# Optimization experiments

Measured on AMD Instinct MI355X. Metric: run time of the kernel, lower is better.

## Reference

```python
import jax, jax.numpy as jnp
import numpy as np

K_GIBBS = 1
LR = 0.01


def _sample_binary(key, probs):
    # relu(sign(p - u)) == 1 iff p > u, else 0
    u = jax.random.uniform(key, probs.shape, dtype=probs.dtype)
    return (probs > u).astype(probs.dtype)


def setup_inputs() -> dict:
    key = jax.random.key(0)
    k1, k2 = jax.random.split(key)
    B, H, Wd, C, hid = 64, 64, 64, 3, 4096
    flat = H * Wd * C  # 12288
    inputs = jax.random.uniform(k1, (B, H, Wd, C), dtype=jnp.float32)
    W = 0.1 * jax.random.normal(k2, (flat, hid), dtype=jnp.float32)  # stddev=0.1 as in build()
    a = jnp.zeros((flat,), jnp.float32)
    b = jnp.zeros((hid,), jnp.float32)
    return {"inputs": inputs, "W": W, "a": a, "b": b}


def reference(inputs, W, a, b):
    B, H, Wd, C = inputs.shape
    flat = H * Wd * C
    vs = inputs.reshape(B, flat)
    keys = jax.random.split(jax.random.key(42), B)
    h0 = jnp.zeros((W.shape[1],), dtype=W.dtype)

    def step(carry, xb):
        W, a, b, h = carry
        v0, key = xb
        kbin, kinit = jax.random.split(key)
        # k Gibbs sampling steps: h = sig(b + W^T v); v = sig(a + W h)
        v = v0
        for _ in range(K_GIBBS):
            h = jax.nn.sigmoid(b + W.T @ v)
            v = jax.nn.sigmoid(a + W @ h)
        # contrastive divergence (rank-1 updates)
        h_bin = _sample_binary(kbin, h)
        h_init = _sample_binary(kinit, jax.nn.sigmoid(b + W.T @ v0))
        W = W + LR * (jnp.outer(v0, h_init) - jnp.outer(v, h_bin))
        a = a + LR * (v0 - v)
        b = b + LR * (h_init - h_bin)
        return (W, a, b, h), None

    (Wf, af, bf, hf), _ = jax.lax.scan(step, (W, a, b, h0), (vs, keys))
    # final self.v.assign(self.v_given_h()) with updated params and last h
    v_final = jax.nn.sigmoid(af + Wf @ hf)
    return v_final.reshape(H, Wd, C)
```

## Files before the change

kernel.cpp:

```cpp
#include <hip/hip_runtime.h>
#include <stdint.h>
#include <math.h>


#define NB   64
#define FLAT 12288
#define HID  4096
#define LRf  0.01f
#define LRd  0.01
#define RNG_MODE 0

#define OFF_KEYS   0u
#define OFF_B      1024u
#define OFF_A      17408u
#define OFF_H      66560u
#define OFF_ALP    82944u
#define OFF_BEP    91136u
#define OFF_G0     99328u
#define OFF_GV     132096u
#define OFF_HIB    164864u
#define OFF_HBB    197632u
#define OFF_C      230400u
#define OFF_V      1278976u
#define OFF_VT     4424704u
#define OFF_V0T    7570432u
#define OFF_HIBC   10716160u
#define OFF_HBBC   10748928u
#define OFF_CPART  1278976u
#define NCH 6

__device__ __forceinline__ void tf(uint32_t k0, uint32_t k1,
                                   uint32_t x0, uint32_t x1,
                                   uint32_t& o0, uint32_t& o1) {
  uint32_t ks[3] = {k0, k1, k0 ^ k1 ^ 0x1BD11BDAu};
  x0 += ks[0]; x1 += ks[1];
  const int R0[4] = {13, 15, 26, 6};
  const int R1[4] = {17, 29, 16, 24};
#pragma unroll
  for (int i = 0; i < 5; ++i) {
    const int* r = (i & 1) ? R1 : R0;
#pragma unroll
    for (int q = 0; q < 4; ++q) {
      x0 += x1;
      x1 = (x1 << r[q]) | (x1 >> (32 - r[q]));
      x1 ^= x0;
    }
    x0 += ks[(i + 1) % 3];
    x1 += ks[(i + 2) % 3] + (uint32_t)(i + 1);
  }
  o0 = x0; o1 = x1;
}

__device__ __forceinline__ float u01(uint32_t bits) {
  uint32_t fb = (bits >> 9) | 0x3f800000u;
  return __uint_as_float(fb) - 1.0f;
}

__global__ void k_setup(const float* a_in, const float* b_in,
                        float* a_cur, float* b_cur, uint32_t* keys4) {
  int gid = blockIdx.x * blockDim.x + threadIdx.x;
  int stride = gridDim.x * blockDim.x;
  for (int i = gid; i < FLAT; i += stride) a_cur[i] = a_in[i];
  for (int i = gid; i < HID; i += stride) b_cur[i] = b_in[i];
  if (gid < NB) {
    uint32_t t = (uint32_t)gid;
    uint32_t kt0, kt1, o0, o1, p0, p1;
#if RNG_MODE == 0
    tf(0u, 42u, 0u, t, kt0, kt1);
    tf(kt0, kt1, 0u, 0u, o0, o1);
    tf(kt0, kt1, 0u, 1u, p0, p1);
    keys4[4 * gid + 0] = o0; keys4[4 * gid + 1] = o1;
    keys4[4 * gid + 2] = p0; keys4[4 * gid + 3] = p1;
#else
    if (t < 32) {
      tf(0u, 42u, 2 * t,     64 + 2 * t, o0, o1); kt0 = o0;
      tf(0u, 42u, 2 * t + 1, 65 + 2 * t, o0, o1); kt1 = o0;
    } else {
      tf(0u, 42u, 2 * t - 64, 2 * t,     o0, o1); kt0 = o1;
      tf(0u, 42u, 2 * t - 63, 2 * t + 1, o0, o1); kt1 = o1;
    }
    uint32_t a0, a1, b0, b1;
    tf(kt0, kt1, 0u, 2u, a0, a1);
    tf(kt0, kt1, 1u, 3u, b0, b1);
    keys4[4 * gid + 0] = a0; keys4[4 * gid + 1] = b0;
    keys4[4 * gid + 2] = a1; keys4[4 * gid + 3] = b1;
#endif
  }
}

__global__ void k_vt(const float* v0all, float* v0T) {
  int i = blockIdx.x * 256 + threadIdx.x;
#pragma unroll 8
  for (int s = 0; s < NB; ++s)
    v0T[(size_t)i * NB + s] = v0all[(size_t)s * FLAT + i];
}

__global__ __launch_bounds__(256) void k_g0(const float* v0all, double* G0) {
  const int t = blockIdx.x, s = blockIdx.y;
  const float4* vs = (const float4*)(v0all + (size_t)s * FLAT);
  const float4* vt = (const float4*)(v0all + (size_t)t * FLAT);
  double acc = 0.0;
  for (int e = threadIdx.x; e < FLAT / 4; e += 256) {
    float4 a = vs[e], b = vt[e];
    acc += (double)a.x * b.x + (double)a.y * b.y +
           (double)a.z * b.z + (double)a.w * b.w;
  }
  for (int m = 32; m; m >>= 1) acc += __shfl_xor(acc, m, 64);
  __shared__ double red[4];
  int wv = threadIdx.x >> 6, lane = threadIdx.x & 63;
  if (lane == 0) red[wv] = acc;
  __syncthreads();
  if (threadIdx.x == 0) G0[s * NB + t] = red[0] + red[1] + red[2] + red[3];
}

__global__ __launch_bounds__(256) void k_cgemm(const float* v0T, const float* W0,
                                               float* Cpart) {
  const int jl = threadIdx.x & 63;
  const int tth = threadIdx.x >> 6;
  const int j0 = blockIdx.x * 64;
  const int ilen = FLAT / NCH;
  const int ibeg = blockIdx.y * ilen, iend = ibeg + ilen;
  __shared__ float lv[64 * 68];
  __shared__ float lw[64 * 68];
  float acc[16];
#pragma unroll
  for (int k = 0; k < 16; ++k) acc[k] = 0.f;
  for (int i0 = ibeg; i0 < iend; i0 += 64) {
    __syncthreads();
    const float4* vsrc = (const float4*)(v0T + (size_t)i0 * NB);
#pragma unroll
    for (int k = 0; k < 4; ++k) {
      int f = threadIdx.x + k * 256;
      int row = f >> 4, c4 = f & 15;
      *(float4*)(&lv[row * 68 + c4 * 4]) = vsrc[f];
    }
#pragma unroll
    for (int k = 0; k < 4; ++k) {
      int f = threadIdx.x + k * 256;
      int row = f >> 4, c4 = f & 15;
      *(float4*)(&lw[row * 68 + c4 * 4]) =
          *(const float4*)(W0 + (size_t)(i0 + row) * HID + j0 + c4 * 4);
    }
    __syncthreads();
#pragma unroll 2
    for (int ii = 0; ii < 64; ++ii) {
      float w = lw[ii * 68 + jl];
      const float* lp = &lv[ii * 68 + tth * 16];
#pragma unroll
      for (int k4 = 0; k4 < 4; ++k4) {
        float4 hv = *(const float4*)(lp + 4 * k4);
        acc[4 * k4 + 0] += w * hv.x;
        acc[4 * k4 + 1] += w * hv.y;
        acc[4 * k4 + 2] += w * hv.z;
        acc[4 * k4 + 3] += w * hv.w;
      }
    }
  }
#pragma unroll
  for (int k = 0; k < 16; ++k)
    Cpart[((size_t)blockIdx.y * NB + tth * 16 + k) * HID + j0 + jl] = acc[k];
}

__global__ void k_creduce(const float* Cpart, float* C) {
  int gid = blockIdx.x * blockDim.x + threadIdx.x;
  if (gid >= NB * HID) return;
  double s = 0.0;
  for (int c = 0; c < NCH; ++c) s += (double)Cpart[(size_t)c * NB * HID + gid];
  C[gid] = (float)s;
}

__global__ __launch_bounds__(256) void k_hbc(int t, const float* Call,
                                             const double* G0, const double* GV,
                                             float* b_cur, float* h_cur,
                                             uint32_t* Hib, uint32_t* Hbb,
                                             uint64_t* HibC, uint64_t* HbbC,
                                             double* alp, double* bep,
                                             const uint32_t* keys4) {
  const int tid = threadIdx.x;
  const int lane = tid & 63, wv = tid >> 6;
  const int j = blockIdx.x * 256 + tid;
  __shared__ double g0c[NB], gvc[NB];
  __shared__ float h_blk[256];
  __shared__ unsigned char ib_blk[256], bb_blk[256];
  __shared__ uint32_t ldsI[NB][8], ldsB[NB][8];
  for (int s = tid; s < NB; s += 256) { g0c[s] = G0[s * NB + t]; gvc[s] = GV[s * NB + t]; }
  for (int idx = tid; idx < t * 8; idx += 256) {
    int s = idx >> 3, w = idx & 7;
    ldsI[s][w] = Hib[s * 128 + blockIdx.x * 8 + w];
    ldsB[s][w] = Hbb[s * 128 + blockIdx.x * 8 + w];
  }
  __syncthreads();
  uint64_t rawI = (t == 0) ? 0ull : HibC[j];
  uint64_t rawB = (t == 0) ? 0ull : HbbC[j];
  const uint64_t mlow = (t == 0) ? 0ull : ((1ull << t) - 1ull);
  uint64_t mi64 = rawI & mlow, mb64 = rawB & mlow;
  double accp = 0.0, accm = 0.0;
  while (mi64) { int s = __builtin_ctzll(mi64); accp += g0c[s]; mi64 &= mi64 - 1; }
  while (mb64) { int s = __builtin_ctzll(mb64); accm += gvc[s]; mb64 &= mb64 - 1; }
  double lg = (double)b_cur[j] + (double)Call[(size_t)t * HID + j] + LRd * (accp - accm);
  float h = (float)(1.0 / (1.0 + exp(-lg)));
  h_cur[j] = h;
  uint32_t o0, o1;
  uint32_t kb0 = keys4[4 * t], kb1 = keys4[4 * t + 1];
  uint32_t ki0 = keys4[4 * t + 2], ki1 = keys4[4 * t + 3];
#if RNG_MODE == 0
  tf(kb0, kb1, 0u, (uint32_t)j, o0, o1); float ub = u01(o0 ^ o1);
  tf(ki0, ki1, 0u, (uint32_t)j, o0, o1); float ui = u01(o0 ^ o1);
#else
  uint32_t m = (uint32_t)(j & (HID / 2 - 1));
  tf(kb0, kb1, m, m + HID / 2, o0, o1); float ub = u01(j < HID / 2 ? o0 : o1);
  tf(ki0, ki1, m, m + HID / 2, o0, o1); float ui = u01(j < HID / 2 ? o0 : o1);
#endif
  bool hb = h > ub, hi = h > ui;
  unsigned long long mb = __ballot(hb), mi = __ballot(hi);
  const int word = j >> 5;
  if (lane == 0) {
    Hbb[t * 128 + word]     = (uint32_t)mb;
    Hbb[t * 128 + word + 1] = (uint32_t)(mb >> 32);
    Hib[t * 128 + word]     = (uint32_t)mi;
    Hib[t * 128 + word + 1] = (uint32_t)(mi >> 32);
  }
  HibC[j] = rawI | ((uint64_t)(hi ? 1 : 0) << t);
  HbbC[j] = rawB | ((uint64_t)(hb ? 1 : 0) << t);
  b_cur[j] += LRf * ((hi ? 1.f : 0.f) - (hb ? 1.f : 0.f));
  h_blk[tid] = h; ib_blk[tid] = hi ? 1 : 0; bb_blk[tid] = hb ? 1 : 0;
  __syncthreads();
  for (int task = wv; task < 2 * (t + 1); task += 4) {
    int s = task >> 1;
    const bool useB = task & 1;
    double p = 0.0;
#pragma unroll
    for (int q = 0; q < 4; ++q) {
      int jj = q * 64 + lane;
      bool on;
      if (s == t) on = (useB ? bb_blk[jj] : ib_blk[jj]) != 0;
      else {
        uint32_t w32 = useB ? ldsB[s][jj >> 5] : ldsI[s][jj >> 5];
        on = (w32 >> (jj & 31)) & 1u;
      }
      if (on) p += (double)h_blk[jj];
    }
    for (int m2 = 32; m2; m2 >>= 1) p += __shfl_xor(p, m2, 64);
    if (lane == 0) {
      if (useB) bep[(size_t)blockIdx.x * NB + s] = p;
      else      alp[(size_t)blockIdx.x * NB + s] = p;
    }
  }
}

__global__ __launch_bounds__(512) void k_gemv(int t, const float* W0,
                                              const float* v0T, const float* h_cur,
                                              const double* alp, const double* bep,
                                              float* a_cur, float* V, float* Vt,
                                              float* out) {
  __shared__ float hs[HID];
  __shared__ double als[NB], bes[NB];
  const int tid = threadIdx.x;
  for (int e = tid; e < HID / 4; e += 512)
    ((float4*)hs)[e] = ((const float4*)h_cur)[e];
  if (tid < NB) {
    double asum = 0.0, bsum = 0.0;
#pragma unroll
    for (int b = 0; b < 16; ++b) {
      asum += alp[(size_t)b * NB + tid];
      bsum += bep[(size_t)b * NB + tid];
    }
    als[tid] = asum; bes[tid] = bsum;
  }
  __syncthreads();
  const int wv = tid >> 6, lane = tid & 63;
  const int row = blockIdx.x * 8 + wv;
  const float4* wr = (const float4*)(W0 + (size_t)row * HID);
  double acc = 0.0;
#pragma unroll
  for (int c = 0; c < 16; ++c) {
    float4 w = wr[c * 64 + lane];
    float4 hh = ((const float4*)hs)[c * 64 + lane];
    acc += (double)w.x * hh.x + (double)w.y * hh.y +
           (double)w.z * hh.z + (double)w.w * hh.w;
  }
  const int smax = (t > NB - 1) ? NB : t;
  if (lane < smax) {
    double c = (double)v0T[(size_t)row * NB + lane] * als[lane]
             - (double)Vt[(size_t)row * NB + lane] * bes[lane];
    acc += LRd * c;
  }
  for (int m = 32; m; m >>= 1) acc += __shfl_xor(acc, m, 64);
  if (lane == 0) {
    double lg = (double)a_cur[row] + acc;
    float v = (float)(1.0 / (1.0 + exp(-lg)));
    if (t == NB) {
      out[row] = v;
    } else {
      V[(size_t)t * FLAT + row] = v;
      Vt[(size_t)row * NB + t] = v;
      a_cur[row] += LRf * (v0T[(size_t)row * NB + t] - v);
    }
  }
}

__global__ void k_gv(int t, const float* v0all, const float* V, double* GV) {
  int tp = t + 1 + blockIdx.x;
  const float4* vt = (const float4*)(V + (size_t)t * FLAT);
  const float4* v0 = (const float4*)(v0all + (size_t)tp * FLAT);
  double acc = 0.0;
  for (int e = threadIdx.x; e < FLAT / 4; e += 256) {
    float4 a = vt[e], b = v0[e];
    acc += (double)a.x * b.x + (double)a.y * b.y +
           (double)a.z * b.z + (double)a.w * b.w;
  }
  for (int m = 32; m; m >>= 1) acc += __shfl_xor(acc, m, 64);
  __shared__ double red[4];
  int wv = threadIdx.x >> 6, lane = threadIdx.x & 63;
  if (lane == 0) red[wv] = acc;
  __syncthreads();
  if (threadIdx.x == 0) GV[t * NB + tp] = red[0] + red[1] + red[2] + red[3];
}

extern "C" void kernel_launch(void* const* d_in, const int* in_sizes, int n_in,
                              void* d_out, int out_size, void* d_ws, size_t ws_size,
                              hipStream_t stream) {
  const float* inputs = (const float*)d_in[0];
  const float* W0     = (const float*)d_in[1];
  const float* a_in   = (const float*)d_in[2];
  const float* b_in   = (const float*)d_in[3];
  float* out = (float*)d_out;

  char* ws = (char*)d_ws;
  uint32_t* keys4 = (uint32_t*)(ws + OFF_KEYS);
  float* b_cur = (float*)(ws + OFF_B);
  float* a_cur = (float*)(ws + OFF_A);
  float* h_cur = (float*)(ws + OFF_H);
  double* alp  = (double*)(ws + OFF_ALP);
  double* bep  = (double*)(ws + OFF_BEP);
  double* G0   = (double*)(ws + OFF_G0);
  double* GV   = (double*)(ws + OFF_GV);
  uint32_t* Hib = (uint32_t*)(ws + OFF_HIB);
  uint32_t* Hbb = (uint32_t*)(ws + OFF_HBB);
  uint64_t* HibC = (uint64_t*)(ws + OFF_HIBC);
  uint64_t* HbbC = (uint64_t*)(ws + OFF_HBBC);
  float* C     = (float*)(ws + OFF_C);
  float* V     = (float*)(ws + OFF_V);
  float* Vt    = (float*)(ws + OFF_VT);
  float* v0T   = (float*)(ws + OFF_V0T);
  float* Cpart = (float*)(ws + OFF_CPART);

  hipLaunchKernelGGL(k_setup, dim3(48), dim3(256), 0, stream,
                     a_in, b_in, a_cur, b_cur, keys4);
  hipLaunchKernelGGL(k_g0, dim3(NB, NB), dim3(256), 0, stream, inputs, G0);
  hipLaunchKernelGGL(k_vt, dim3(FLAT / 256), dim3(256), 0, stream, inputs, v0T);
  hipLaunchKernelGGL(k_cgemm, dim3(HID / 64, NCH), dim3(256), 0, stream,
                     v0T, W0, Cpart);
  hipLaunchKernelGGL(k_creduce, dim3((NB * HID + 255) / 256), dim3(256), 0,
                     stream, Cpart, C);

  for (int t = 0; t < NB; ++t) {
    hipLaunchKernelGGL(k_hbc, dim3(HID / 256), dim3(256), 0, stream,
                       t, C, G0, GV, b_cur, h_cur, Hib, Hbb, HibC, HbbC,
                       alp, bep, keys4);
    hipLaunchKernelGGL(k_gemv, dim3(FLAT / 8), dim3(512), 0, stream,
                       t, W0, v0T, h_cur, alp, bep, a_cur, V, Vt, out);
    if (t < NB - 1)
      hipLaunchKernelGGL(k_gv, dim3(NB - 1 - t), dim3(256), 0, stream,
                         t, inputs, V, GV);
  }
  hipLaunchKernelGGL(k_gemv, dim3(FLAT / 8), dim3(512), 0, stream,
                     NB, W0, v0T, h_cur, alp, bep, a_cur, V, Vt, out);
}
```

Baseline: 4.042 ms.

## Fuse GV dot products into gemv epilogue and reduce partials in k_hbc

Removes the per-step k_gv kernel. k_gemv now computes per-block partial products of the new v with every v0 column and writes them to Gpart. The next k_hbc reduces those partials into GV and gvc, which saves one launch per step and a separate full reread of V and the inputs. It also retiles k_cgemm to 32-column tiles with 8 accumulators and raises NCH to 8, giving more blocks. The cost is extra shared memory and a syncthreads in gemv, plus a 1536-entry column reduction done redundantly inside each k_hbc block.

```diff
diff --git a/kernel.cpp b/kernel.cpp
--- a/kernel.cpp
+++ b/kernel.cpp
@@ -9,6 +9,7 @@
 #define LRf  0.01f
 #define LRd  0.01
 #define RNG_MODE 0
+#define GEMV_BLOCKS (FLAT / 8)
 
 #define OFF_KEYS   0u
 #define OFF_B      1024u
@@ -21,13 +22,13 @@
 #define OFF_HIB    164864u
 #define OFF_HBB    197632u
 #define OFF_C      230400u
-#define OFF_V      1278976u
 #define OFF_VT     4424704u
 #define OFF_V0T    7570432u
 #define OFF_HIBC   10716160u
 #define OFF_HBBC   10748928u
-#define OFF_CPART  1278976u
-#define NCH 6
+#define OFF_CPART  10781696u
+#define NCH 8
+#define OFF_GPART  19170304u
 
 __device__ __forceinline__ void tf(uint32_t k0, uint32_t k1,
                                    uint32_t x0, uint32_t x1,
@@ -115,16 +116,16 @@
 
 __global__ __launch_bounds__(256) void k_cgemm(const float* v0T, const float* W0,
                                                float* Cpart) {
-  const int jl = threadIdx.x & 63;
-  const int tth = threadIdx.x >> 6;
-  const int j0 = blockIdx.x * 64;
+  const int jl = threadIdx.x & 31;
+  const int tth = threadIdx.x >> 5;
+  const int j0 = blockIdx.x * 32;
   const int ilen = FLAT / NCH;
   const int ibeg = blockIdx.y * ilen, iend = ibeg + ilen;
   __shared__ float lv[64 * 68];
-  __shared__ float lw[64 * 68];
-  float acc[16];
-#pragma unroll
-  for (int k = 0; k < 16; ++k) acc[k] = 0.f;
+  __shared__ float lw[64 * 36];
+  float acc[8];
+#pragma unroll
+  for (int k = 0; k < 8; ++k) acc[k] = 0.f;
   for (int i0 = ibeg; i0 < iend; i0 += 64) {
     __syncthreads();
     const float4* vsrc = (const float4*)(v0T + (size_t)i0 * NB);
@@ -135,30 +136,28 @@
       *(float4*)(&lv[row * 68 + c4 * 4]) = vsrc[f];
     }
 #pragma unroll
-    for (int k = 0; k < 4; ++k) {
+    for (int k = 0; k < 2; ++k) {
       int f = threadIdx.x + k * 256;
-      int row = f >> 4, c4 = f & 15;
-      *(float4*)(&lw[row * 68 + c4 * 4]) =
+      int row = f >> 3, c4 = f & 7;
+      *(float4*)(&lw[row * 36 + c4 * 4]) =
           *(const float4*)(W0 + (size_t)(i0 + row) * HID + j0 + c4 * 4);
     }
     __syncthreads();
 #pragma unroll 2
     for (int ii = 0; ii < 64; ++ii) {
-      float w = lw[ii * 68 + jl];
-      const float* lp = &lv[ii * 68 + tth * 16];
-#pragma unroll
-      for (int k4 = 0; k4 < 4; ++k4) {
-        float4 hv = *(const float4*)(lp + 4 * k4);
-        acc[4 * k4 + 0] += w * hv.x;
-        acc[4 * k4 + 1] += w * hv.y;
-        acc[4 * k4 + 2] += w * hv.z;
-        acc[4 * k4 + 3] += w * hv.w;
-      }
-    }
-  }
-#pragma unroll
-  for (int k = 0; k < 16; ++k)
-    Cpart[((size_t)blockIdx.y * NB + tth * 16 + k) * HID + j0 + jl] = acc[k];
+      float w = lw[ii * 36 + jl];
+      const float* lp = &lv[ii * 68 + tth * 8];
+      float4 h0 = *(const float4*)(lp);
+      float4 h1 = *(const float4*)(lp + 4);
+      acc[0] += w * h0.x; acc[1] += w * h0.y;
+      acc[2] += w * h0.z; acc[3] += w * h0.w;
+      acc[4] += w * h1.x; acc[5] += w * h1.y;
+      acc[6] += w * h1.z; acc[7] += w * h1.w;
+    }
+  }
+#pragma unroll
+  for (int k = 0; k < 8; ++k)
+    Cpart[((size_t)blockIdx.y * NB + tth * 8 + k) * HID + j0 + jl] = acc[k];
 }
 
 __global__ void k_creduce(const float* Cpart, float* C) {
@@ -170,7 +169,8 @@
 }
 
 __global__ __launch_bounds__(256) void k_hbc(int t, const float* Call,
-                                             const double* G0, const double* GV,
+                                             const double* G0, double* GV,
+                                             const double* Gpart,
                                              float* b_cur, float* h_cur,
                                              uint32_t* Hib, uint32_t* Hbb,
                                              uint64_t* HibC, uint64_t* HbbC,
@@ -180,6 +180,7 @@
   const int lane = tid & 63, wv = tid >> 6;
   const int j = blockIdx.x * 256 + tid;
   __shared__ double g0c[NB], gvc[NB];
+  __shared__ double colred[4];
   __shared__ float h_blk[256];
   __shared__ unsigned char ib_blk[256], bb_blk[256];
   __shared__ uint32_t ldsI[NB][8], ldsB[NB][8];
@@ -188,6 +189,25 @@
     int s = idx >> 3, w = idx & 7;
     ldsI[s][w] = Hib[s * 128 + blockIdx.x * 8 + w];
     ldsB[s][w] = Hbb[s * 128 + blockIdx.x * 8 + w];
+  }
+  if (t > 0) {
+#pragma unroll 1
+    for (int c = 0; c < 5; ++c) {
+      int tp = (c == 4) ? t : ((int)blockIdx.x + 16 * c);
+      if (c < 4 && tp <= t) continue;
+      double ps = 0.0;
+      for (int b = tid; b < GEMV_BLOCKS; b += 256)
+        ps += Gpart[(size_t)b * NB + tp];
+      for (int m = 32; m; m >>= 1) ps += __shfl_xor(ps, m, 64);
+      if (lane == 0) colred[wv] = ps;
+      __syncthreads();
+      if (tid == 0) {
+        double tot = colred[0] + colred[1] + colred[2] + colred[3];
+        if (c == 4) gvc[t - 1] = tot;
+        else GV[(size_t)(t - 1) * NB + tp] = tot;
+      }
+      __syncthreads();
+    }
   }
   __syncthreads();
   uint64_t rawI = (t == 0) ? 0ull : HibC[j];
@@ -251,10 +271,11 @@
 __global__ __launch_bounds__(512) void k_gemv(int t, const float* W0,
                                               const float* v0T, const float* h_cur,
                                               const double* alp, const double* bep,
-                                              float* a_cur, float* V, float* Vt,
-                                              float* out) {
+                                              float* a_cur, float* Vt,
+                                              double* Gpart, float* out) {
   __shared__ float hs[HID];
   __shared__ double als[NB], bes[NB];
+  __shared__ double gp[8][NB];
   const int tid = threadIdx.x;
   for (int e = tid; e < HID / 4; e += 512)
     ((float4*)hs)[e] = ((const float4*)h_cur)[e];
@@ -280,41 +301,30 @@
            (double)w.z * hh.z + (double)w.w * hh.w;
   }
   const int smax = (t > NB - 1) ? NB : t;
+  double v0l = (double)v0T[(size_t)row * NB + lane];
   if (lane < smax) {
-    double c = (double)v0T[(size_t)row * NB + lane] * als[lane]
-             - (double)Vt[(size_t)row * NB + lane] * bes[lane];
-    acc += LRd * c;
+    acc += LRd * (v0l * als[lane]
+                  - (double)Vt[(size_t)row * NB + lane] * bes[lane]);
   }
   for (int m = 32; m; m >>= 1) acc += __shfl_xor(acc, m, 64);
-  if (lane == 0) {
-    double lg = (double)a_cur[row] + acc;
-    float v = (float)(1.0 / (1.0 + exp(-lg)));
-    if (t == NB) {
-      out[row] = v;
-    } else {
-      V[(size_t)t * FLAT + row] = v;
-      Vt[(size_t)row * NB + t] = v;
-      a_cur[row] += LRf * (v0T[(size_t)row * NB + t] - v);
-    }
-  }
-}
-
-__global__ void k_gv(int t, const float* v0all, const float* V, double* GV) {
-  int tp = t + 1 + blockIdx.x;
-  const float4* vt = (const float4*)(V + (size_t)t * FLAT);
-  const float4* v0 = (const float4*)(v0all + (size_t)tp * FLAT);
-  double acc = 0.0;
-  for (int e = threadIdx.x; e < FLAT / 4; e += 256) {
-    float4 a = vt[e], b = v0[e];
-    acc += (double)a.x * b.x + (double)a.y * b.y +
-           (double)a.z * b.z + (double)a.w * b.w;
-  }
-  for (int m = 32; m; m >>= 1) acc += __shfl_xor(acc, m, 64);
-  __shared__ double red[4];
-  int wv = threadIdx.x >> 6, lane = threadIdx.x & 63;
-  if (lane == 0) red[wv] = acc;
-  __syncthreads();
-  if (threadIdx.x == 0) GV[t * NB + tp] = red[0] + red[1] + red[2] + red[3];
+  double lg = (double)a_cur[row] + acc;
+  float vv = (float)(1.0 / (1.0 + exp(-lg)));
+  if (t == NB) {
+    if (lane == 0) out[row] = vv;
+  } else {
+    if (lane == 0) {
+      Vt[(size_t)row * NB + t] = vv;
+      a_cur[row] += LRf * (v0T[(size_t)row * NB + t] - vv);
+    }
+    if (t < NB - 1) gp[wv][lane] = (double)vv * v0l;
+  }
+  __syncthreads();
+  if (t < NB - 1 && tid < NB) {
+    double s = 0.0;
+#pragma unroll
+    for (int w = 0; w < 8; ++w) s += gp[w][tid];
+    Gpart[(size_t)blockIdx.x * NB + tid] = s;
+  }
 }
 
 extern "C" void kernel_launch(void* const* d_in, const int* in_sizes, int n_in,
@@ -340,30 +350,27 @@
   uint64_t* HibC = (uint64_t*)(ws + OFF_HIBC);
   uint64_t* HbbC = (uint64_t*)(ws + OFF_HBBC);
   float* C     = (float*)(ws + OFF_C);
-  float* V     = (float*)(ws + OFF_V);
   float* Vt    = (float*)(ws + OFF_VT);
   float* v0T   = (float*)(ws + OFF_V0T);
   float* Cpart = (float*)(ws + OFF_CPART);
+  double* Gpart = (double*)(ws + OFF_GPART);
 
   hipLaunchKernelGGL(k_setup, dim3(48), dim3(256), 0, stream,
                      a_in, b_in, a_cur, b_cur, keys4);
   hipLaunchKernelGGL(k_g0, dim3(NB, NB), dim3(256), 0, stream, inputs, G0);
   hipLaunchKernelGGL(k_vt, dim3(FLAT / 256), dim3(256), 0, stream, inputs, v0T);
-  hipLaunchKernelGGL(k_cgemm, dim3(HID / 64, NCH), dim3(256), 0, stream,
+  hipLaunchKernelGGL(k_cgemm, dim3(HID / 32, NCH), dim3(256), 0, stream,
                      v0T, W0, Cpart);
   hipLaunchKernelGGL(k_creduce, dim3((NB * HID + 255) / 256), dim3(256), 0,
                      stream, Cpart, C);
 
   for (int t = 0; t < NB; ++t) {
     hipLaunchKernelGGL(k_hbc, dim3(HID / 256), dim3(256), 0, stream,
-                       t, C, G0, GV, b_cur, h_cur, Hib, Hbb, HibC, HbbC,
+                       t, C, G0, GV, Gpart, b_cur, h_cur, Hib, Hbb, HibC, HbbC,
                        alp, bep, keys4);
-    hipLaunchKernelGGL(k_gemv, dim3(FLAT / 8), dim3(512), 0, stream,
-                       t, W0, v0T, h_cur, alp, bep, a_cur, V, Vt, out);
-    if (t < NB - 1)
-      hipLaunchKernelGGL(k_gv, dim3(NB - 1 - t), dim3(256), 0, stream,
-                         t, inputs, V, GV);
-  }
-  hipLaunchKernelGGL(k_gemv, dim3(FLAT / 8), dim3(512), 0, stream,
-                     NB, W0, v0T, h_cur, alp, bep, a_cur, V, Vt, out);
-}
+    hipLaunchKernelGGL(k_gemv, dim3(GEMV_BLOCKS), dim3(512), 0, stream,
+                       t, W0, v0T, h_cur, alp, bep, a_cur, Vt, Gpart, out);
+  }
+  hipLaunchKernelGGL(k_gemv, dim3(GEMV_BLOCKS), dim3(512), 0, stream,
+                     NB, W0, v0T, h_cur, alp, bep, a_cur, Vt, Gpart, out);
+}
```

Result: slower. 4.127 ms (+2.1%).
